# Kernel tuning notes

Measured on AMD Instinct MI355X. Metric: run time of the kernel, lower is better.

## Reference

```python
import jax, jax.numpy as jnp
import numpy as np

B, S, V, F = 8, 500, 100, 5          # batch, n_samples(=500 hard-coded), n_vertices, n_feat
NT, NR = 4, 3                         # n_thetas, n_rhos
K = NT * NR                           # gaussian kernels = 12
MAX_RHO = 12.0
N_ROT = 1
EPS = 1e-5
TWO_PI = 2.0 * np.pi


def _initial_coords():
    # faithful to compute_initial_coordinates(): rho-major flattening
    grid_rho = np.linspace(0.0, MAX_RHO, NR + 1)[1:]
    grid_theta = np.linspace(0.0, TWO_PI, NT + 1)[:-1]
    r_, t_ = np.meshgrid(grid_rho, grid_theta)
    return r_.T.flatten().astype(np.float32), t_.T.flatten().astype(np.float32)


def setup_inputs() -> dict:
    key = jax.random.key(0)
    ks = jax.random.split(key, 8)
    input_feat = jax.random.normal(ks[0], (B, S, V, F), jnp.float32)
    rho_coords = jax.random.uniform(ks[1], (B, S, V, 1), jnp.float32) * MAX_RHO
    theta_coords = jax.random.uniform(ks[2], (B, S, V, 1), jnp.float32) * TWO_PI
    mask = (jax.random.uniform(ks[3], (B, S, V, 1)) > 0.1).astype(jnp.float32)
    mr, mt = _initial_coords()
    mu_rho = jnp.tile(jnp.asarray(mr)[None, :], (F, 1))          # [F,K]
    mu_theta = jnp.tile(jnp.asarray(mt)[None, :], (F, 1))        # [F,K]
    sigma_rho = jnp.full((F, K), MAX_RHO / 8.0, jnp.float32)
    sigma_theta = jnp.ones((F, K), jnp.float32)
    W_conv = jax.random.normal(ks[4], (F, K, K), jnp.float32) * (1.0 / np.sqrt(K))
    b_conv = jnp.zeros((F, K), jnp.float32)
    W2 = jax.random.normal(ks[5], (F * K, K), jnp.float32) * (1.0 / np.sqrt(F * K))
    b2 = jnp.zeros((K,), jnp.float32)
    W3 = jax.random.normal(ks[6], (K, F), jnp.float32) * (1.0 / np.sqrt(K))
    b3 = jnp.zeros((F,), jnp.float32)
    W4 = jax.random.normal(ks[7], (F, 3), jnp.float32) * (1.0 / np.sqrt(F))
    b4 = jnp.zeros((3,), jnp.float32)
    return dict(input_feat=input_feat, rho_coords=rho_coords, theta_coords=theta_coords,
                mask=mask, mu_rho=mu_rho, sigma_rho=sigma_rho, mu_theta=mu_theta,
                sigma_theta=sigma_theta, W_conv=W_conv, b_conv=b_conv,
                W2=W2, b2=b2, W3=W3, b3=b3, W4=W4, b4=b4)


def reference(input_feat, rho_coords, theta_coords, mask, mu_rho, sigma_rho,
              mu_theta, sigma_theta, W_conv, b_conv, W2, b2, W3, b3, W4, b4):
    rho = rho_coords[..., 0]    # [B,S,V]
    th0 = theta_coords[..., 0]  # [B,S,V]
    # Gaussian in rho, per feature channel f and kernel k -> [B,F,S,V,K]
    g_rho = jnp.exp(-(rho[:, None, :, :, None] - mu_rho[None, :, None, None, :]) ** 2
                    / (sigma_rho[None, :, None, None, :] ** 2 + EPS))
    m = mask[:, None, :, :, :]  # [B,1,S,V,1]
    convs = []
    for r in range(N_ROT):
        th = jnp.mod(th0 + r * TWO_PI / N_ROT, TWO_PI)
        g_th = jnp.exp(-(th[:, None, :, :, None] - mu_theta[None, :, None, None, :]) ** 2
                       / (sigma_theta[None, :, None, None, :] ** 2 + EPS))
        g = g_rho * g_th * m                                   # [B,F,S,V,K]
        # NOTE: source normalizes over axis 1 (the n_samples/patch axis), faithful here (axis=2 in BFSVK)
        g = g / (jnp.sum(g, axis=2, keepdims=True) + EPS)
        desc = jnp.einsum('bfsvk,bsvf->bfsk', g, input_feat)   # sum over vertices
        convs.append(jnp.einsum('bfsk,fkj->bfsj', desc, W_conv) + b_conv[None, :, None, :])
    conv = jax.nn.relu(jnp.max(jnp.stack(convs, 0), 0))        # [B,F,S,K]
    gd = conv.transpose(0, 2, 1, 3).reshape(B, S, F * K)       # stack axis=2 order (F then K)
    h = jax.nn.relu(gd @ W2 + b2)
    h = jax.nn.relu(h @ W3 + b3)
    return jax.nn.softmax(h @ W4 + b4, axis=-1)                # [B,S,3]
```

## Files before the change

### kernel.cpp

```cpp
#include <hip/hip_runtime.h>
#include <math.h>

namespace {
constexpr int Bc = 8, Sc = 500, Vc = 100, Fc = 5, Kc = 12, FKc = 60;
constexpr int BV = Bc * Vc;
constexpr int NDEN = BV * FKc;
constexpr int VG = 25;
constexpr float EPSc = 1e-5f;
}

__device__ __forceinline__ void gauss_consts(
    const float* __restrict__ mu_rho, const float* __restrict__ sigma_rho,
    const float* __restrict__ mu_theta, const float* __restrict__ sigma_theta,
    int fk,
    float& nr1, float& nr2, float& nr3,
    float& nt1, float& nt2, float& nt3)
{
    float mr = mu_rho[fk],  sr = sigma_rho[fk];
    float mt = mu_theta[fk], st = sigma_theta[fk];
    float isr = 1.0f / (sr * sr + EPSc);
    float ist = 1.0f / (st * st + EPSc);
    nr1 = -isr; nr2 = 2.0f * isr * mr; nr3 = -(isr * mr) * mr;
    nt1 = -ist; nt2 = 2.0f * ist * mt; nt3 = -(ist * mt) * mt;
}

__global__ __launch_bounds__(64) void k_denom_partial(
    const float* __restrict__ rho, const float* __restrict__ theta,
    const float* __restrict__ mask,
    const float* __restrict__ mu_rho, const float* __restrict__ sigma_rho,
    const float* __restrict__ mu_theta, const float* __restrict__ sigma_theta,
    float* __restrict__ partial, int chunk)
{
    const int c  = blockIdx.x;
    const int b  = blockIdx.y;
    const int wg = blockIdx.z;
    const int lane = threadIdx.x;
    const int fk = lane < FKc ? lane : FKc - 1;
    const int v0 = wg * VG;

    float nr1, nr2, nr3, nt1, nt2, nt3;
    gauss_consts(mu_rho, sigma_rho, mu_theta, sigma_theta, fk,
                 nr1, nr2, nr3, nt1, nt2, nt3);

    const int s0 = c * chunk;
    const int s1 = min(Sc, s0 + chunk);

    float acc[VG];
#pragma unroll
    for (int i = 0; i < VG; ++i) acc[i] = 0.0f;

    const size_t base = (size_t)b * Sc * Vc + v0;
    for (int s = s0; s < s1; ++s) {
        const float* rp = rho   + base + (size_t)s * Vc;
        const float* tp = theta + base + (size_t)s * Vc;
        const float* mp = mask  + base + (size_t)s * Vc;
#pragma unroll
        for (int vi = 0; vi < VG; ++vi) {
            float r = rp[vi], t = tp[vi], m = mp[vi];
            float ar = __fmaf_rn(__fmaf_rn(nr1, r, nr2), r, nr3);
            float at = __fmaf_rn(__fmaf_rn(nt1, t, nt2), t, nt3 + ar);
            acc[vi] = __fmaf_rn(__expf(at), m, acc[vi]);
        }
    }

    float* pp = partial + (size_t)c * NDEN + ((size_t)b * Vc + v0) * FKc;
    if (lane < FKc) {
#pragma unroll
        for (int vi = 0; vi < VG; ++vi)
            pp[(size_t)vi * FKc + lane] = acc[vi];
    }
}

__global__ __launch_bounds__(256) void k_inv(
    const float* __restrict__ partial, float* __restrict__ inv_denom, int SCH)
{
    const int i = blockIdx.x * 256 + threadIdx.x;
    if (i >= NDEN) return;
    float s = 0.0f;
    for (int c = 0; c < SCH; ++c)
        s += partial[(size_t)c * NDEN + i];
    inv_denom[i] = 1.0f / (s + EPSc);
}

__global__ __launch_bounds__(256) void k_main(
    const float* __restrict__ feat, const float* __restrict__ rho,
    const float* __restrict__ theta, const float* __restrict__ mask,
    const float* __restrict__ mu_rho, const float* __restrict__ sigma_rho,
    const float* __restrict__ mu_theta, const float* __restrict__ sigma_theta,
    const float* __restrict__ Wc, const float* __restrict__ bc,
    const float* __restrict__ W2, const float* __restrict__ b2,
    const float* __restrict__ W3, const float* __restrict__ b3,
    const float* __restrict__ W4, const float* __restrict__ b4,
    const float* __restrict__ inv_denom,
    float* __restrict__ out)
{
    const int bs = blockIdx.x;
    const int b = bs / Sc;
    const int tid = threadIdx.x;
    const int w = tid >> 6;
    const int lane = tid & 63;
    const int fk = lane < FKc ? lane : FKc - 1;
    const int f = fk / Kc;

    __shared__ float lds_id[Vc * FKc];
    __shared__ float lds_feat[Vc * Fc];
    __shared__ float lds_red[4][FKc];
    __shared__ float lds_gd[FKc];
    __shared__ float lds_h1[Kc];
    __shared__ float lds_h2[Fc];
    __shared__ float lds_logit[3];

    const float4* idp = (const float4*)(inv_denom + (size_t)b * Vc * FKc);
    float4* ldp = (float4*)lds_id;
    for (int i = tid; i < Vc * FKc / 4; i += 256) ldp[i] = idp[i];
    const float* frow = feat + (size_t)bs * Vc * Fc;
    for (int i = tid; i < Vc * Fc; i += 256) lds_feat[i] = frow[i];

    float nr1, nr2, nr3, nt1, nt2, nt3;
    gauss_consts(mu_rho, sigma_rho, mu_theta, sigma_theta, fk,
                 nr1, nr2, nr3, nt1, nt2, nt3);

    __syncthreads();

    const size_t base_sv = (size_t)bs * Vc + w * VG;
    float acc = 0.0f;
#pragma unroll
    for (int vi = 0; vi < VG; ++vi) {
        const int v = w * VG + vi;
        float r = rho[base_sv + vi];
        float t = theta[base_sv + vi];
        float m = mask[base_sv + vi];
        float id = lds_id[v * FKc + fk];
        float fv = lds_feat[v * Fc + f];
        float ar = __fmaf_rn(__fmaf_rn(nr1, r, nr2), r, nr3);
        float at = __fmaf_rn(__fmaf_rn(nt1, t, nt2), t, nt3 + ar);
        acc = __fmaf_rn(__expf(at) * m * id, fv, acc);
    }
    if (lane < FKc) lds_red[w][lane] = acc;
    __syncthreads();

    if (tid < FKc) {
        float d0 = lds_red[0][tid] + lds_red[1][tid] +
                   lds_red[2][tid] + lds_red[3][tid];
        lds_gd[tid] = d0;
    }
    __syncthreads();
    float gd_val = 0.0f;
    if (tid < FKc) {
        const int ff = tid / Kc, j = tid % Kc;
        float sum = bc[tid];
#pragma unroll
        for (int k = 0; k < Kc; ++k)
            sum = __fmaf_rn(lds_gd[ff * Kc + k],
                            Wc[ff * Kc * Kc + k * Kc + j], sum);
        gd_val = fmaxf(sum, 0.0f);
    }
    __syncthreads();
    if (tid < FKc) lds_gd[tid] = gd_val;
    __syncthreads();

    if (tid < Kc) {
        float sum = b2[tid];
#pragma unroll
        for (int i = 0; i < FKc; ++i)
            sum = __fmaf_rn(lds_gd[i], W2[i * Kc + tid], sum);
        lds_h1[tid] = fmaxf(sum, 0.0f);
    }
    __syncthreads();

    if (tid < Fc) {
        float sum = b3[tid];
#pragma unroll
        for (int i = 0; i < Kc; ++i)
            sum = __fmaf_rn(lds_h1[i], W3[i * Fc + tid], sum);
        lds_h2[tid] = fmaxf(sum, 0.0f);
    }
    __syncthreads();

    if (tid < 3) {
        float sum = b4[tid];
#pragma unroll
        for (int i = 0; i < Fc; ++i)
            sum = __fmaf_rn(lds_h2[i], W4[i * 3 + tid], sum);
        lds_logit[tid] = sum;
    }
    __syncthreads();

    if (tid == 0) {
        float l0 = lds_logit[0], l1 = lds_logit[1], l2 = lds_logit[2];
        float mx = fmaxf(l0, fmaxf(l1, l2));
        float e0 = __expf(l0 - mx), e1 = __expf(l1 - mx), e2 = __expf(l2 - mx);
        float inv = 1.0f / (e0 + e1 + e2);
        out[(size_t)bs * 3 + 0] = e0 * inv;
        out[(size_t)bs * 3 + 1] = e1 * inv;
        out[(size_t)bs * 3 + 2] = e2 * inv;
    }
}

extern "C" void kernel_launch(void* const* d_in, const int* in_sizes, int n_in,
                              void* d_out, int out_size, void* d_ws, size_t ws_size,
                              hipStream_t stream) {
    const float* feat     = (const float*)d_in[0];
    const float* rho      = (const float*)d_in[1];
    const float* theta    = (const float*)d_in[2];
    const float* mask     = (const float*)d_in[3];
    const float* mu_rho   = (const float*)d_in[4];
    const float* sig_rho  = (const float*)d_in[5];
    const float* mu_theta = (const float*)d_in[6];
    const float* sig_th   = (const float*)d_in[7];
    const float* Wc       = (const float*)d_in[8];
    const float* bc       = (const float*)d_in[9];
    const float* W2       = (const float*)d_in[10];
    const float* b2       = (const float*)d_in[11];
    const float* W3       = (const float*)d_in[12];
    const float* b3       = (const float*)d_in[13];
    const float* W4       = (const float*)d_in[14];
    const float* b4       = (const float*)d_in[15];

    float* inv_denom = (float*)d_ws;
    const size_t inv_bytes = (size_t)NDEN * 4;
    size_t rem = ws_size > inv_bytes ? ws_size - inv_bytes : 0;
    int SCH = (int)(rem / inv_bytes);
    if (SCH > 50) SCH = 50;
    float* partial;
    if (SCH < 1) { SCH = 1; partial = inv_denom; }
    else partial = inv_denom + NDEN;
    const int chunk = (Sc + SCH - 1) / SCH;

    k_denom_partial<<<dim3(SCH, Bc, 4), 64, 0, stream>>>(
        rho, theta, mask, mu_rho, sig_rho, mu_theta, sig_th, partial, chunk);

    k_inv<<<(NDEN + 255) / 256, 256, 0, stream>>>(partial, inv_denom, SCH);

    k_main<<<Bc * Sc, 256, 0, stream>>>(
        feat, rho, theta, mask, mu_rho, sig_rho, mu_theta, sig_th,
        Wc, bc, W2, b2, W3, b3, W4, b4, inv_denom, (float*)d_out);
}
```

Before: 140.6 us.

## Shrink main kernel to one wavefront per sample and stage weights in LDS

The main kernel now runs one 64-lane wavefront per (b,s) instead of four. That lane loops over all 100 vertices and reads inverse denominators directly from global/L2 instead of staging 24KB into LDS. This removes the cross-wave reduction, most barriers and the large LDS footprint, and puts rho/theta/mask, W_conv and W2 into LDS. The denominator split also goes up to 100 chunks for more parallelism in the first kernel. The trade-off is a longer serial loop per lane with 100 exps and more global loads of inv_denom per block.

```diff
diff --git a/kernel.cpp b/kernel.cpp
--- a/kernel.cpp
+++ b/kernel.cpp
@@ -77,12 +77,13 @@
     const int i = blockIdx.x * 256 + threadIdx.x;
     if (i >= NDEN) return;
     float s = 0.0f;
+#pragma unroll 4
     for (int c = 0; c < SCH; ++c)
         s += partial[(size_t)c * NDEN + i];
     inv_denom[i] = 1.0f / (s + EPSc);
 }
 
-__global__ __launch_bounds__(256) void k_main(
+__global__ __launch_bounds__(64) void k_main(
     const float* __restrict__ feat, const float* __restrict__ rho,
     const float* __restrict__ theta, const float* __restrict__ mask,
     const float* __restrict__ mu_rho, const float* __restrict__ sigma_rho,
@@ -96,25 +97,46 @@
 {
     const int bs = blockIdx.x;
     const int b = bs / Sc;
-    const int tid = threadIdx.x;
-    const int w = tid >> 6;
-    const int lane = tid & 63;
+    const int lane = threadIdx.x;
     const int fk = lane < FKc ? lane : FKc - 1;
     const int f = fk / Kc;
 
-    __shared__ float lds_id[Vc * FKc];
     __shared__ float lds_feat[Vc * Fc];
-    __shared__ float lds_red[4][FKc];
+    __shared__ float lds_r[Vc];
+    __shared__ float lds_t[Vc];
+    __shared__ float lds_m[Vc];
+    __shared__ float lds_wc[Fc * Kc * Kc];
+    __shared__ float lds_w2[FKc * Kc];
+    __shared__ float lds_desc[FKc];
     __shared__ float lds_gd[FKc];
     __shared__ float lds_h1[Kc];
     __shared__ float lds_h2[Fc];
     __shared__ float lds_logit[3];
 
-    const float4* idp = (const float4*)(inv_denom + (size_t)b * Vc * FKc);
-    float4* ldp = (float4*)lds_id;
-    for (int i = tid; i < Vc * FKc / 4; i += 256) ldp[i] = idp[i];
-    const float* frow = feat + (size_t)bs * Vc * Fc;
-    for (int i = tid; i < Vc * Fc; i += 256) lds_feat[i] = frow[i];
+    {
+        const float4* s_f = (const float4*)(feat + (size_t)bs * Vc * Fc);
+        float4* d_f = (float4*)lds_feat;
+#pragma unroll
+        for (int i = lane; i < Vc * Fc / 4; i += 64) d_f[i] = s_f[i];
+
+        const float4* s_r = (const float4*)(rho   + (size_t)bs * Vc);
+        const float4* s_t = (const float4*)(theta + (size_t)bs * Vc);
+        const float4* s_m = (const float4*)(mask  + (size_t)bs * Vc);
+        if (lane < Vc / 4) {
+            ((float4*)lds_r)[lane] = s_r[lane];
+            ((float4*)lds_t)[lane] = s_t[lane];
+            ((float4*)lds_m)[lane] = s_m[lane];
+        }
+        const float4* s_wc = (const float4*)Wc;
+        const float4* s_w2 = (const float4*)W2;
+        float4* d_wc = (float4*)lds_wc;
+        float4* d_w2 = (float4*)lds_w2;
+#pragma unroll
+        for (int i = lane; i < Fc * Kc * Kc / 4; i += 64) {
+            d_wc[i] = s_wc[i];
+            d_w2[i] = s_w2[i];
+        }
+    }
 
     float nr1, nr2, nr3, nt1, nt2, nt3;
     gauss_consts(mu_rho, sigma_rho, mu_theta, sigma_theta, fk,
@@ -122,78 +144,67 @@
 
     __syncthreads();
 
-    const size_t base_sv = (size_t)bs * Vc + w * VG;
+    const size_t base_bv = (size_t)b * Vc;
     float acc = 0.0f;
-#pragma unroll
-    for (int vi = 0; vi < VG; ++vi) {
-        const int v = w * VG + vi;
-        float r = rho[base_sv + vi];
-        float t = theta[base_sv + vi];
-        float m = mask[base_sv + vi];
-        float id = lds_id[v * FKc + fk];
+#pragma unroll 10
+    for (int v = 0; v < Vc; ++v) {
+        float id = inv_denom[(base_bv + v) * FKc + fk];
+        float r = lds_r[v];
+        float t = lds_t[v];
+        float m = lds_m[v];
         float fv = lds_feat[v * Fc + f];
         float ar = __fmaf_rn(__fmaf_rn(nr1, r, nr2), r, nr3);
         float at = __fmaf_rn(__fmaf_rn(nt1, t, nt2), t, nt3 + ar);
         acc = __fmaf_rn(__expf(at) * m * id, fv, acc);
     }
-    if (lane < FKc) lds_red[w][lane] = acc;
-    __syncthreads();
-
-    if (tid < FKc) {
-        float d0 = lds_red[0][tid] + lds_red[1][tid] +
-                   lds_red[2][tid] + lds_red[3][tid];
-        lds_gd[tid] = d0;
-    }
-    __syncthreads();
-    float gd_val = 0.0f;
-    if (tid < FKc) {
-        const int ff = tid / Kc, j = tid % Kc;
-        float sum = bc[tid];
+    if (lane < FKc) lds_desc[lane] = acc;
+    __syncthreads();
+
+    if (lane < FKc) {
+        const int ff = lane / Kc, j = lane % Kc;
+        float sum = bc[lane];
 #pragma unroll
         for (int k = 0; k < Kc; ++k)
-            sum = __fmaf_rn(lds_gd[ff * Kc + k],
-                            Wc[ff * Kc * Kc + k * Kc + j], sum);
-        gd_val = fmaxf(sum, 0.0f);
-    }
-    __syncthreads();
-    if (tid < FKc) lds_gd[tid] = gd_val;
-    __syncthreads();
-
-    if (tid < Kc) {
-        float sum = b2[tid];
+            sum = __fmaf_rn(lds_desc[ff * Kc + k],
+                            lds_wc[ff * Kc * Kc + k * Kc + j], sum);
+        lds_gd[lane] = fmaxf(sum, 0.0f);
+    }
+    __syncthreads();
+
+    if (lane < Kc) {
+        float sum = b2[lane];
 #pragma unroll
         for (int i = 0; i < FKc; ++i)
-            sum = __fmaf_rn(lds_gd[i], W2[i * Kc + tid], sum);
-        lds_h1[tid] = fmaxf(sum, 0.0f);
-    }
-    __syncthreads();
-
-    if (tid < Fc) {
-        float sum = b3[tid];
+            sum = __fmaf_rn(lds_gd[i], lds_w2[i * Kc + lane], sum);
+        lds_h1[lane] = fmaxf(sum, 0.0f);
+    }
+    __syncthreads();
+
+    if (lane < Fc) {
+        float sum = b3[lane];
 #pragma unroll
         for (int i = 0; i < Kc; ++i)
-            sum = __fmaf_rn(lds_h1[i], W3[i * Fc + tid], sum);
-        lds_h2[tid] = fmaxf(sum, 0.0f);
-    }
-    __syncthreads();
-
-    if (tid < 3) {
-        float sum = b4[tid];
+            sum = __fmaf_rn(lds_h1[i], W3[i * Fc + lane], sum);
+        lds_h2[lane] = fmaxf(sum, 0.0f);
+    }
+    __syncthreads();
+
+    if (lane < 3) {
+        float sum = b4[lane];
 #pragma unroll
         for (int i = 0; i < Fc; ++i)
-            sum = __fmaf_rn(lds_h2[i], W4[i * 3 + tid], sum);
-        lds_logit[tid] = sum;
-    }
-    __syncthreads();
-
-    if (tid == 0) {
+            sum = __fmaf_rn(lds_h2[i], W4[i * 3 + lane], sum);
+        lds_logit[lane] = sum;
+    }
+    __syncthreads();
+
+    if (lane < 3) {
         float l0 = lds_logit[0], l1 = lds_logit[1], l2 = lds_logit[2];
         float mx = fmaxf(l0, fmaxf(l1, l2));
         float e0 = __expf(l0 - mx), e1 = __expf(l1 - mx), e2 = __expf(l2 - mx);
         float inv = 1.0f / (e0 + e1 + e2);
-        out[(size_t)bs * 3 + 0] = e0 * inv;
-        out[(size_t)bs * 3 + 1] = e1 * inv;
-        out[(size_t)bs * 3 + 2] = e2 * inv;
+        float mine = lane == 0 ? e0 : (lane == 1 ? e1 : e2);
+        out[(size_t)bs * 3 + lane] = mine * inv;
     }
 }
 
@@ -221,7 +232,7 @@
     const size_t inv_bytes = (size_t)NDEN * 4;
     size_t rem = ws_size > inv_bytes ? ws_size - inv_bytes : 0;
     int SCH = (int)(rem / inv_bytes);
-    if (SCH > 50) SCH = 50;
+    if (SCH > 100) SCH = 100;
     float* partial;
     if (SCH < 1) { SCH = 1; partial = inv_denom; }
     else partial = inv_denom + NDEN;
@@ -232,7 +243,7 @@
 
     k_inv<<<(NDEN + 255) / 256, 256, 0, stream>>>(partial, inv_denom, SCH);
 
-    k_main<<<Bc * Sc, 256, 0, stream>>>(
+    k_main<<<Bc * Sc, 64, 0, stream>>>(
         feat, rho, theta, mask, mu_rho, sig_rho, mu_theta, sig_th,
         Wc, bc, W2, b2, W3, b3, W4, b4, inv_denom, (float*)d_out);
 }
```

After: 126.8 us. 1.11x faster.
